# Performance work log

Hardware: AMD Instinct MI355X
Metric: run time of the kernel (lower is better)

## Reference

```python
import jax, jax.numpy as jnp
import numpy as np

N_SPH = 7
N_RAD = 6
CUTOFF = 5.0
P = 5  # envelope exponent
E = 500000
T = 2000000

# ---- numpy-side precompute of spherical Bessel roots & normalizers ----
# matches sympy bessel_basis(n,k): basis[l][j] = N_{l,j} * j_l(z_{l,j} * x)

def _sph_jn_np(t, l):
    t = np.asarray(t, dtype=np.float64)
    j0 = np.sin(t) / t
    if l == 0:
        return j0
    j1 = np.sin(t) / t**2 - np.cos(t) / t
    for i in range(2, l + 1):
        j0, j1 = j1, (2 * i - 1) / t * j1 - j0
    return j1


def _jn_zeros(n, k):
    # k-th zeros of spherical bessel j_l for l=0..n-1, via interlacing + bisection
    nz = k + n - 1
    zeros = np.zeros((n, nz))
    zeros[0] = np.arange(1, nz + 1) * np.pi  # zeros of j_0
    for l in range(1, n):
        for i in range(nz - l):
            a, b = zeros[l - 1, i], zeros[l - 1, i + 1]
            fa = _sph_jn_np(a, l)
            for _ in range(80):
                m = 0.5 * (a + b)
                fm = _sph_jn_np(m, l)
                if fa * fm <= 0:
                    b = m
                else:
                    a, fa = m, fm
            zeros[l, i] = 0.5 * (a + b)
    return zeros[:, :k]

_Z = _jn_zeros(N_SPH, N_RAD)  # [n, k]
_NORM = np.sqrt(2.0) / np.abs(np.stack([_sph_jn_np(_Z[l], l + 1) for l in range(N_SPH)]))
FREQ = jnp.asarray(_Z, dtype=jnp.float32)   # [n, k]
NORM = jnp.asarray(_NORM, dtype=jnp.float32)  # [n, k]
# real sph harm (m=0): Y_l(theta) = sqrt((2l+1)/4pi) * P_l(cos theta)
Y_COEF = jnp.asarray(np.sqrt((2 * np.arange(N_SPH) + 1) / (4 * np.pi)), dtype=jnp.float32)


def _sph_jn(t, l):
    j0 = jnp.sin(t) / t
    if l == 0:
        return j0
    j1 = jnp.sin(t) / t**2 - jnp.cos(t) / t
    for i in range(2, l + 1):
        j0, j1 = j1, (2 * i - 1) / t * j1 - j0
    return j1


def _forward(dist, angle, idx_kj):
    n, k = N_SPH, N_RAD
    x = dist / CUTOFF  # [E]
    # radial basis: [E, n*k], layout l-major / j-minor like torch stack order
    rbf = jnp.concatenate(
        [NORM[l] * _sph_jn(x[:, None] * FREQ[l], l) for l in range(n)], axis=1)
    # envelope (DimeNet variant: no cutoff masking)
    a = -(P + 1) * (P + 2) / 2.0
    b = float(P * (P + 2))
    c = -P * (P + 1) / 2.0
    xp = x**P
    env = 1.0 / x + a * xp + b * xp * x + c * xp * x * x
    rbf = env[:, None] * rbf
    # angular basis via Legendre recurrence on cos(theta)
    cth = jnp.cos(angle)
    Ps = [jnp.ones_like(cth), cth]
    for l in range(2, n):
        Ps.append(((2 * l - 1) * cth * Ps[-1] - (l - 1) * Ps[-2]) / l)
    cbf = jnp.stack([Y_COEF[l] * Ps[l] for l in range(n)], axis=1)  # [T, n]
    out = (rbf[idx_kj].reshape(-1, n, k) * cbf[:, :, None]).reshape(-1, n * k)
    return out


def setup_inputs() -> dict:
    key = jax.random.key(0)
    k1, k2, k3 = jax.random.split(key, 3)
    # distances kept away from 0 (envelope has 1/x term)
    dist = jax.random.uniform(k1, (E,), jnp.float32, 0.1, 1.0) * CUTOFF
    angle = jax.random.uniform(k2, (T,), jnp.float32, 0.0, float(np.pi))
    idx_kj = jax.random.randint(k3, (T,), 0, E)
    return {"dist": dist, "angle": angle, "idx_kj": idx_kj}


def reference(dist, angle, idx_kj):
    return _forward(dist, angle, idx_kj)
```

## Files before the change

kernel.cpp:

```cpp
#include <hip/hip_runtime.h>
#include <hip/hip_bf16.h>
#include <cmath>

#define N_SPH 7
#define N_RAD 6
#define NC (N_SPH * N_RAD)
#define INV_CUTOFF 0.2f

typedef float f2 __attribute__((ext_vector_type(2)));
typedef float f4 __attribute__((ext_vector_type(4)));

static constexpr int M_TAB[NC] = {
    2,  4,  6,  8,  10, 12,
    3,  5,  7,  9,  11, 13,
    4,  6,  8,  10, 12, 14,
    4,  7,  9,  11, 13, 15,
    5,  7,  10, 12, 14, 16,
    6,  8,  10, 13, 15, 17,
    7,  9,  11, 13, 15, 18};

struct BesselConsts {
    float freq[NC];
    float norm[NC];
    float deltaf[NC];
    float ycoef[N_SPH];
    double deltad[NC];
};

static double h_sph_jn(double t, int l) {
    double j0 = sin(t) / t;
    if (l == 0) return j0;
    double j1 = sin(t) / (t * t) - cos(t) / t;
    for (int i = 2; i <= l; i++) {
        double j2 = (2.0 * i - 1.0) / t * j1 - j0;
        j0 = j1; j1 = j2;
    }
    return j1;
}

static void compute_consts(BesselConsts* bc) {
    const int n = N_SPH, k = N_RAD, nz = N_RAD + N_SPH - 1;
    const double PI = 3.14159265358979323846;
    const double PI_2 = 1.57079632679489661923;
    double zeros[N_SPH][12];
    for (int i = 0; i < nz; i++) zeros[0][i] = (i + 1) * PI;
    for (int l = 1; l < n; l++) {
        for (int i = 0; i < nz - l; i++) {
            double a = zeros[l - 1][i], b = zeros[l - 1][i + 1];
            double fa = h_sph_jn(a, l);
            for (int it = 0; it < 80; it++) {
                double m = 0.5 * (a + b);
                double fm = h_sph_jn(m, l);
                if (fa * fm <= 0.0) { b = m; } else { a = m; fa = fm; }
            }
            zeros[l][i] = 0.5 * (a + b);
        }
    }
    for (int l = 0; l < n; l++)
        for (int j = 0; j < k; j++) {
            const int c = l * k + j;
            bc->freq[c] = (float)zeros[l][j];
            bc->norm[c] =
                (float)(sqrt(2.0) / fabs(h_sph_jn(zeros[l][j], l + 1)));
            double dd = zeros[l][j] - (double)M_TAB[c] * PI_2;
            bc->deltad[c] = dd;
            bc->deltaf[c] = (float)dd;
        }
    for (int l = 0; l < n; l++)
        bc->ycoef[l] = (float)sqrt((2.0 * l + 1.0) / (4.0 * PI));
}

template <int L, int C_>
__device__ __forceinline__ void elem32(float x, float env, float Sf, float Cf,
                                       const float* yP, float* strow,
                                       const BesselConsts& bc) {
    float tt = x * bc.freq[C_];
    float u = x * bc.deltaf[C_];
    float v = u * u;
    float su = u * fmaf(v, fmaf(v, fmaf(v, fmaf(v, fmaf(v, -2.5052108e-8f,
                    2.7557319e-6f), -1.9841270e-4f), 8.3333333e-3f),
                    -1.6666667e-1f), 1.0f);
    float cu = fmaf(v, fmaf(v, fmaf(v, fmaf(v, fmaf(v, fmaf(v, 2.0876757e-9f,
                    -2.7557319e-7f), 2.4801587e-5f), -1.3888889e-3f),
                    4.1666667e-2f), -0.5f), 1.0f);
    float s = fmaf(Sf, cu, Cf * su);
    float co = fmaf(Cf, cu, -(Sf * su));
    float r = __builtin_amdgcn_rcpf(tt);
    r = r * fmaf(-tt, r, 2.0f);
    float jv;
    float j0 = s * r;
    if constexpr (L == 0) {
        jv = j0;
    } else {
        float j1 = fmaf(s, r, -co) * r;
#pragma unroll
        for (int i = 2; i <= L; ++i) {
            float j2 = fmaf((2.0f * i - 1.0f) * r, j1, -j0);
            j0 = j1; j1 = j2;
        }
        jv = j1;
    }
    strow[C_] = yP[L] * (env * bc.norm[C_] * jv);
}

template <int L, int C_>
__device__ __forceinline__ void elem64(float x, double xd, float env,
                                       double Sd, double Cd, const float* yP,
                                       float* strow, const BesselConsts& bc) {
    float tt = x * bc.freq[C_];
    double u = xd * bc.deltad[C_];
    double v = u * u;
    double su = u * fma(v, fma(v, fma(v, fma(v, fma(v, -1.0 / 39916800.0,
                     1.0 / 362880.0), -1.0 / 5040.0), 1.0 / 120.0),
                     -1.0 / 6.0), 1.0);
    double cu = fma(v, fma(v, fma(v, fma(v, fma(v, fma(v, 1.0 / 479001600.0,
                     -1.0 / 3628800.0), 1.0 / 40320.0), -1.0 / 720.0),
                     1.0 / 24.0), -0.5), 1.0);
    double s = fma(Sd, cu, Cd * su);
    double co = fma(Cd, cu, -(Sd * su));
    double td = (double)tt;
    float rf = __builtin_amdgcn_rcpf(tt);
    double r = (double)rf;
    r = r * fma(-td, r, 2.0);
    double j0 = s * r;
    double j1 = fma(s, r, -co) * r;
#pragma unroll
    for (int i = 2; i <= L; ++i) {
        double j2 = fma((2.0 * i - 1.0) * r, j1, -j0);
        j0 = j1; j1 = j2;
    }
    strow[C_] = yP[L] * (env * bc.norm[C_] * (float)j1);
}

__global__ __launch_bounds__(256) void fused_row_kernel(
    const float* __restrict__ dist, const float* __restrict__ angle,
    const int* __restrict__ idx, float* __restrict__ out, int T_,
    BesselConsts bc) {
    __shared__ __align__(16) float stage[256 * NC];
    const int tix = threadIdx.x;
    const int t0 = blockIdx.x * 256;
    const int t = t0 + tix;
    const bool valid = t < T_;

    float x = 0.5f, cth = 0.0f;
    if (valid) {
        x = dist[idx[t]] * INV_CUTOFF;
        cth = cosf(angle[t]);
    }
    float xp = x * x * x * x * x;
    float env = 1.0f / x + xp * (-21.0f + x * (35.0f - 15.0f * x));
    float P[N_SPH];
    P[0] = 1.0f;
    P[1] = cth;
#pragma unroll
    for (int l = 2; l < N_SPH; ++l)
        P[l] = ((2 * l - 1) * cth * P[l - 1] - (l - 1) * P[l - 2]) *
               (1.0f / (float)l);
    float yP[N_SPH];
#pragma unroll
    for (int l = 0; l < N_SPH; ++l) yP[l] = bc.ycoef[l] * P[l];

    double xd = (double)x;
    double th = xd * 1.57079632679489661923;
    double w = th * th;
    double s1 = th * fma(w, fma(w, fma(w, fma(w, fma(w, fma(w,
                     1.0 / 6227020800.0, -1.0 / 39916800.0), 1.0 / 362880.0),
                     -1.0 / 5040.0), 1.0 / 120.0), -1.0 / 6.0), 1.0);
    double c1 = fma(w, fma(w, fma(w, fma(w, fma(w, fma(w, fma(w,
                     -1.0 / 87178291200.0, 1.0 / 479001600.0),
                     -1.0 / 3628800.0), 1.0 / 40320.0), -1.0 / 720.0),
                     1.0 / 24.0), -0.5), 1.0);
    double S = s1, C = c1;

    float* strow = &stage[tix * NC];

#define STEP() do { double Sn = fma(S, c1, C * s1); \
                    C = fma(C, c1, -(S * s1)); S = Sn; } while (0)
#define E32(L_, C_) do { float Sf = (float)S, Cf = (float)C; \
                         elem32<L_, C_>(x, env, Sf, Cf, yP, strow, bc); } while (0)
#define E64(L_, C_) elem64<L_, C_>(x, xd, env, S, C, yP, strow, bc)

    STEP();  E32(0, 0);
    STEP();  E32(1, 6);
    STEP();  E32(0, 1);  E32(2, 12); E32(3, 18);
    STEP();  E32(1, 7);  E64(4, 24);
    STEP();  E32(0, 2);  E32(2, 13); E64(5, 30);
    STEP();  E32(1, 8);  E32(3, 19); E64(4, 25); E64(6, 36);
    STEP();  E32(0, 3);  E32(2, 14); E64(5, 31);
    STEP();  E32(1, 9);  E32(3, 20); E64(6, 37);
    STEP();  E32(0, 4);  E32(2, 15); E64(4, 26); E64(5, 32);
    STEP();  E32(1, 10); E32(3, 21); E64(6, 38);
    STEP();  E32(0, 5);  E32(2, 16); E64(4, 27);
    STEP();  E32(1, 11); E32(3, 22); E64(5, 33); E64(6, 39);
    STEP();  E32(2, 17); E64(4, 28);
    STEP();  E32(3, 23); E64(5, 34); E64(6, 40);
    STEP();  E64(4, 29);
    STEP();  E64(5, 35);
    STEP();  E64(6, 41);
#undef STEP
#undef E32
#undef E64

    __syncthreads();

    const int rows = min(256, T_ - t0);
    const int nelem = rows * NC;
    const int n4 = nelem >> 2;
    const size_t base = (size_t)t0 * NC;
#pragma unroll
    for (int it = 0; it < 11; ++it) {
        int i = it * 256 + tix;
        if (i < n4) {
            f4 v = *reinterpret_cast<const f4*>(&stage[4 * i]);
            __builtin_nontemporal_store(
                v, reinterpret_cast<f4*>(out + base + 4 * (size_t)i));
        }
    }
    for (int i = n4 * 4 + tix; i < nelem; i += 256)
        __builtin_nontemporal_store(stage[i], out + base + i);
}

extern "C" void kernel_launch(void* const* d_in, const int* in_sizes, int n_in,
                              void* d_out, int out_size, void* d_ws,
                              size_t ws_size, hipStream_t stream) {
    const float* dist = (const float*)d_in[0];
    const float* angle = (const float*)d_in[1];
    const int* idx = (const int*)d_in[2];
    float* out = (float*)d_out;

    int E_ = in_sizes[0];
    int T_ = in_sizes[1];
    (void)E_; (void)d_ws; (void)ws_size;

    BesselConsts bc;
    compute_consts(&bc);

    fused_row_kernel<<<(T_ + 255) / 256, 256, 0, stream>>>(dist, angle, idx,
                                                           out, T_, bc);
}
```

Before: 374.2 us.

## Stage results in fp16 LDS, shorten polynomials, move most orders to fp32

The kernel now keeps its shared-memory staging buffer in _Float16 and widens values back to float when writing output. This halves LDS use so more blocks fit per CU, and a launch-bounds hint of 5 blocks is added. The sin/cos correction polynomials in the fp32 path are shortened, and most l=4..6 Bessel elements move from the double path to fp32. Together these reduce ALU and fp64 work, but they lower output precision to fp16 (about 3 significant digits) and risk exceeding the tolerance, especially for the high-order recurrences now done in float.

After: 376.3 us. No clear change (+0.6%).

```diff
diff --git a/kernel.cpp b/kernel.cpp
--- a/kernel.cpp
+++ b/kernel.cpp
@@ -9,6 +9,7 @@
 
 typedef float f2 __attribute__((ext_vector_type(2)));
 typedef float f4 __attribute__((ext_vector_type(4)));
+typedef _Float16 h8 __attribute__((ext_vector_type(8)));
 
 static constexpr int M_TAB[NC] = {
     2,  4,  6,  8,  10, 12,
@@ -72,17 +73,15 @@
 
 template <int L, int C_>
 __device__ __forceinline__ void elem32(float x, float env, float Sf, float Cf,
-                                       const float* yP, float* strow,
+                                       const float* yP, _Float16* strow,
                                        const BesselConsts& bc) {
     float tt = x * bc.freq[C_];
     float u = x * bc.deltaf[C_];
     float v = u * u;
-    float su = u * fmaf(v, fmaf(v, fmaf(v, fmaf(v, fmaf(v, -2.5052108e-8f,
-                    2.7557319e-6f), -1.9841270e-4f), 8.3333333e-3f),
-                    -1.6666667e-1f), 1.0f);
-    float cu = fmaf(v, fmaf(v, fmaf(v, fmaf(v, fmaf(v, fmaf(v, 2.0876757e-9f,
-                    -2.7557319e-7f), 2.4801587e-5f), -1.3888889e-3f),
-                    4.1666667e-2f), -0.5f), 1.0f);
+    float su = u * fmaf(v, fmaf(v, fmaf(v, -1.9841270e-4f, 8.3333333e-3f),
+                                 -1.6666667e-1f), 1.0f);
+    float cu = fmaf(v, fmaf(v, fmaf(v, fmaf(v, 2.4801587e-5f, -1.3888889e-3f),
+                                    4.1666667e-2f), -0.5f), 1.0f);
     float s = fmaf(Sf, cu, Cf * su);
     float co = fmaf(Cf, cu, -(Sf * su));
     float r = __builtin_amdgcn_rcpf(tt);
@@ -100,13 +99,14 @@
         }
         jv = j1;
     }
-    strow[C_] = yP[L] * (env * bc.norm[C_] * jv);
+    strow[C_] = (_Float16)(yP[L] * (env * bc.norm[C_] * jv));
 }
 
 template <int L, int C_>
 __device__ __forceinline__ void elem64(float x, double xd, float env,
                                        double Sd, double Cd, const float* yP,
-                                       float* strow, const BesselConsts& bc) {
+                                       _Float16* strow,
+                                       const BesselConsts& bc) {
     float tt = x * bc.freq[C_];
     double u = xd * bc.deltad[C_];
     double v = u * u;
@@ -129,14 +129,14 @@
         double j2 = fma((2.0 * i - 1.0) * r, j1, -j0);
         j0 = j1; j1 = j2;
     }
-    strow[C_] = yP[L] * (env * bc.norm[C_] * (float)j1);
-}
-
-__global__ __launch_bounds__(256) void fused_row_kernel(
+    strow[C_] = (_Float16)(yP[L] * (env * bc.norm[C_] * (float)j1));
+}
+
+__global__ __launch_bounds__(256, 5) void fused_row_kernel(
     const float* __restrict__ dist, const float* __restrict__ angle,
     const int* __restrict__ idx, float* __restrict__ out, int T_,
     BesselConsts bc) {
-    __shared__ __align__(16) float stage[256 * NC];
+    __shared__ __align__(16) _Float16 stage[256 * NC];
     const int tix = threadIdx.x;
     const int t0 = blockIdx.x * 256;
     const int t = t0 + tix;
@@ -172,7 +172,7 @@
                      1.0 / 24.0), -0.5), 1.0);
     double S = s1, C = c1;
 
-    float* strow = &stage[tix * NC];
+    _Float16* strow = &stage[tix * NC];
 
 #define STEP() do { double Sn = fma(S, c1, C * s1); \
                     C = fma(C, c1, -(S * s1)); S = Sn; } while (0)
@@ -185,18 +185,18 @@
     STEP();  E32(0, 1);  E32(2, 12); E32(3, 18);
     STEP();  E32(1, 7);  E64(4, 24);
     STEP();  E32(0, 2);  E32(2, 13); E64(5, 30);
-    STEP();  E32(1, 8);  E32(3, 19); E64(4, 25); E64(6, 36);
-    STEP();  E32(0, 3);  E32(2, 14); E64(5, 31);
+    STEP();  E32(1, 8);  E32(3, 19); E32(4, 25); E64(6, 36);
+    STEP();  E32(0, 3);  E32(2, 14); E32(5, 31);
     STEP();  E32(1, 9);  E32(3, 20); E64(6, 37);
-    STEP();  E32(0, 4);  E32(2, 15); E64(4, 26); E64(5, 32);
-    STEP();  E32(1, 10); E32(3, 21); E64(6, 38);
-    STEP();  E32(0, 5);  E32(2, 16); E64(4, 27);
-    STEP();  E32(1, 11); E32(3, 22); E64(5, 33); E64(6, 39);
-    STEP();  E32(2, 17); E64(4, 28);
-    STEP();  E32(3, 23); E64(5, 34); E64(6, 40);
-    STEP();  E64(4, 29);
-    STEP();  E64(5, 35);
-    STEP();  E64(6, 41);
+    STEP();  E32(0, 4);  E32(2, 15); E32(4, 26); E32(5, 32);
+    STEP();  E32(1, 10); E32(3, 21); E32(6, 38);
+    STEP();  E32(0, 5);  E32(2, 16); E32(4, 27);
+    STEP();  E32(1, 11); E32(3, 22); E32(5, 33); E32(6, 39);
+    STEP();  E32(2, 17); E32(4, 28);
+    STEP();  E32(3, 23); E32(5, 34); E32(6, 40);
+    STEP();  E32(4, 29);
+    STEP();  E32(5, 35);
+    STEP();  E32(6, 41);
 #undef STEP
 #undef E32
 #undef E64
@@ -205,19 +205,23 @@
 
     const int rows = min(256, T_ - t0);
     const int nelem = rows * NC;
-    const int n4 = nelem >> 2;
+    const int n8 = nelem >> 3;
     const size_t base = (size_t)t0 * NC;
 #pragma unroll
-    for (int it = 0; it < 11; ++it) {
+    for (int it = 0; it < 6; ++it) {
         int i = it * 256 + tix;
-        if (i < n4) {
-            f4 v = *reinterpret_cast<const f4*>(&stage[4 * i]);
+        if (i < n8) {
+            h8 hv = *reinterpret_cast<const h8*>(&stage[8 * i]);
+            f4 lo = {(float)hv[0], (float)hv[1], (float)hv[2], (float)hv[3]};
+            f4 hi = {(float)hv[4], (float)hv[5], (float)hv[6], (float)hv[7]};
             __builtin_nontemporal_store(
-                v, reinterpret_cast<f4*>(out + base + 4 * (size_t)i));
-        }
-    }
-    for (int i = n4 * 4 + tix; i < nelem; i += 256)
-        __builtin_nontemporal_store(stage[i], out + base + i);
+                lo, reinterpret_cast<f4*>(out + base + 8 * (size_t)i));
+            __builtin_nontemporal_store(
+                hi, reinterpret_cast<f4*>(out + base + 8 * (size_t)i + 4));
+        }
+    }
+    for (int i = n8 * 8 + tix; i < nelem; i += 256)
+        __builtin_nontemporal_store((float)stage[i], out + base + i);
 }
 
 extern "C" void kernel_launch(void* const* d_in, const int* in_sizes, int n_in,
```
